# Kernel optimization log

Hardware: AMD Instinct MI355X
Metric: run time of the kernel (lower is better)

Reference implementation:

```python
import jax, jax.numpy as jnp
import numpy as np

B, T, HID = 2, 2048, 2048
NH, NKV = 16, 8
NOPE, ROPE = 128, 64
HD = NOPE + ROPE  # 192
VD = 128
KV_RANK, Q_RANK = 512, 1536
EPS = 1e-6
THETA = 10000.0
GROUPS = NH // NKV


def rmsnorm(x, w):
    var = jnp.mean(x * x, axis=-1, keepdims=True)
    return x * jax.lax.rsqrt(var + EPS) * w


def rope_cos_sin(seq_len, dtype):
    inv_freq = 1.0 / (THETA ** (jnp.arange(0, ROPE, 2, dtype=jnp.float32) / ROPE))
    t = jnp.arange(seq_len, dtype=jnp.float32)
    freqs = jnp.outer(t, inv_freq)
    emb = jnp.concatenate([freqs, freqs], axis=-1)  # [T, ROPE]
    return jnp.cos(emb).astype(dtype)[None, :, None, :], jnp.sin(emb).astype(dtype)[None, :, None, :]


def rotate_half(x):
    x1, x2 = x[..., : x.shape[-1] // 2], x[..., x.shape[-1] // 2 :]
    return jnp.concatenate([-x2, x1], axis=-1)


def setup_inputs() -> dict:
    key = jax.random.key(0)
    ks = jax.random.split(key, 7)
    s = 0.02
    return {
        "hidden_states": jax.random.normal(ks[0], (B, T, HID), jnp.float32),
        "q_a_w": jax.random.normal(ks[1], (HID, Q_RANK), jnp.float32) * s,
        "q_a_ln_w": jnp.ones((Q_RANK,), jnp.float32),
        "q_b_w": jax.random.normal(ks[2], (Q_RANK, NH * HD), jnp.float32) * s,
        "kv_a_w": jax.random.normal(ks[3], (HID, KV_RANK + NKV * ROPE), jnp.float32) * s,
        "kv_a_ln_w": jnp.ones((KV_RANK,), jnp.float32),
        "kv_b_w": jax.random.normal(ks[4], (KV_RANK, NKV * (NOPE + VD)), jnp.float32) * s,
        "o_w": jax.random.normal(ks[5], (NH * VD, HID), jnp.float32) * s,
    }


def reference(hidden_states, q_a_w, q_a_ln_w, q_b_w, kv_a_w, kv_a_ln_w, kv_b_w, o_w):
    x = hidden_states
    # Q low-rank path: a_proj -> RMSNorm -> b_proj
    q = rmsnorm(x @ q_a_w, q_a_ln_w) @ q_b_w
    q = q.reshape(B, T, NH, HD)
    q_nope, q_rope = q[..., :NOPE], q[..., NOPE:]
    # KV low-rank + decoupled rope key
    kv_raw = x @ kv_a_w
    kv_latent = rmsnorm(kv_raw[..., :KV_RANK], kv_a_ln_w)
    k_rope = kv_raw[..., KV_RANK:].reshape(B, T, NKV, ROPE)
    kv = (kv_latent @ kv_b_w).reshape(B, T, NKV, NOPE + VD)
    k_nope, v = kv[..., :NOPE], kv[..., NOPE:]
    # partial RoPE on rope slice only
    cos, sin = rope_cos_sin(T, x.dtype)
    q_rope = q_rope * cos + rotate_half(q_rope) * sin
    k_rope = k_rope * cos + rotate_half(k_rope) * sin
    q_full = jnp.concatenate([q_nope, q_rope], axis=-1)  # [B,T,NH,HD]
    k_full = jnp.concatenate([k_nope, k_rope], axis=-1)  # [B,T,NKV,HD]
    # GQA expansion (repeat_interleave over head dim)
    k_full = jnp.repeat(k_full, GROUPS, axis=2)  # [B,T,NH,HD]
    v_full = jnp.repeat(v, GROUPS, axis=2)       # [B,T,NH,VD]
    scale = HD ** -0.5
    scores = jnp.einsum("bqhd,bkhd->bhqk", q_full, k_full) * scale
    probs = jax.nn.softmax(scores, axis=-1)
    attn = jnp.einsum("bhqk,bkhd->bqhd", probs, v_full)
    out = attn.reshape(B, T, NH * VD) @ o_w
    return out
```

## Files before the change

kernel.cpp:

```cpp
#include <hip/hip_runtime.h>

using u16 = unsigned short;
using u32 = unsigned int;

typedef float f32x4 __attribute__((ext_vector_type(4)));
typedef __bf16 bf16x8 __attribute__((ext_vector_type(8)));
typedef u32 u32x2 __attribute__((ext_vector_type(2)));

__device__ __forceinline__ u16 f2bf(float f){
  u32 u = __builtin_bit_cast(u32, f);
  u32 r = (u + 0x7fffu + ((u >> 16) & 1u)) >> 16;
  return (u16)r;
}
__device__ __forceinline__ float bf2f(u16 h){
  u32 u = ((u32)h) << 16;
  return __builtin_bit_cast(float, u);
}
__device__ __forceinline__ void gl2lds16(const void* g, void* l){
  __builtin_amdgcn_global_load_lds((const __attribute__((address_space(1))) u32*)g,
                                   (__attribute__((address_space(3))) u32*)l, 16, 0, 0);
}
__device__ __forceinline__ int swz24(int ck, int r){ return (ck & 24) | ((ck ^ r) & 7); }
__device__ __forceinline__ u32 cvtpk_bf16(float a, float b){
  u32 r; asm("v_cvt_pk_bf16_f32 %0, %1, %2" : "=v"(r) : "v"(a), "v"(b)); return r;
}
__device__ __forceinline__ void mfma16(f32x4& acc, u32x2 a, u32x2 b){
  asm("v_mfma_f32_16x16x16_bf16 %0, %1, %2, %0" : "+v"(acc) : "v"(a), "v"(b));
}

__global__ __launch_bounds__(256) void cvt_f32_bf16(const float* __restrict__ in,
                                                    u16* __restrict__ out, long n){
  long i = ((long)blockIdx.x*256 + threadIdx.x)*4;
  if (i >= n) return;
  float4 v = *(const float4*)(in + i);
  u16 o[4] = { f2bf(v.x), f2bf(v.y), f2bf(v.z), f2bf(v.w) };
  *(ushort4*)(out + i) = *(ushort4*)o;
}

__global__ __launch_bounds__(256) void transpose_w(const float* __restrict__ in,
                                                   u16* __restrict__ out, int K, int N){
  __shared__ float tile[32][33];
  int n0 = blockIdx.x*32, k0 = blockIdx.y*32;
  int tx = threadIdx.x, ty = threadIdx.y;
  for (int i = ty; i < 32; i += 8)
    tile[i][tx] = in[(size_t)(k0+i)*N + n0+tx];
  __syncthreads();
  for (int i = ty; i < 32; i += 8)
    out[(size_t)(n0+i)*K + k0+tx] = f2bf(tile[tx][i]);
}

__global__ __launch_bounds__(256) void rope_tables(float* __restrict__ cosT, float* __restrict__ sinT){
  int idx = blockIdx.x*256 + threadIdx.x;
  int t = idx >> 5, d = idx & 31;
  double inv = pow(10000.0, -(double)d / 32.0);
  double a = (double)t * inv;
  cosT[idx] = (float)cos(a);
  sinT[idx] = (float)sin(a);
}

template<int OUT_BF16>
__global__ __launch_bounds__(256) void gemm_bt(const u16* __restrict__ A,
                                               const u16* __restrict__ Bt,
                                               void* __restrict__ Cout,
                                               int M, int N, int K, float cscale){
  __shared__ u16 As[128*32];
  __shared__ u16 Bs[128*32];
  const int tid = threadIdx.x, lane = tid & 63, wave = tid >> 6;
  const int m0 = blockIdx.y*128, n0 = blockIdx.x*128;
  const int wm = (wave >> 1)*64, wn = (wave & 1)*64;
  const int g = lane >> 4, lr = lane & 15;
  f32x4 acc[4][4] = {};
  const int sr = (wave*2)*16 + (lane >> 2);
  const int sc = (lane & 3)*8;
  for (int k0 = 0; k0 < K; k0 += 32){
    __syncthreads();
    #pragma unroll
    for (int i = 0; i < 2; i++){
      int c = wave*2 + i;
      int r = sr + i*16;
      gl2lds16(A  + (size_t)(m0+r)*K + k0 + sc, (char*)As + c*1024);
      gl2lds16(Bt + (size_t)(n0+r)*K + k0 + sc, (char*)Bs + c*1024);
    }
    __syncthreads();
    bf16x8 af[4], bfr[4];
    #pragma unroll
    for (int mi = 0; mi < 4; mi++) af[mi]  = *reinterpret_cast<const bf16x8*>(&As[(wm+mi*16+lr)*32 + g*8]);
    #pragma unroll
    for (int ni = 0; ni < 4; ni++) bfr[ni] = *reinterpret_cast<const bf16x8*>(&Bs[(wn+ni*16+lr)*32 + g*8]);
    #pragma unroll
    for (int mi = 0; mi < 4; mi++)
      #pragma unroll
      for (int ni = 0; ni < 4; ni++)
        acc[mi][ni] = __builtin_amdgcn_mfma_f32_16x16x32_bf16(af[mi], bfr[ni], acc[mi][ni], 0,0,0);
  }
  #pragma unroll
  for (int mi = 0; mi < 4; mi++)
    #pragma unroll
    for (int ni = 0; ni < 4; ni++)
      #pragma unroll
      for (int r = 0; r < 4; r++){
        int row = m0 + wm + mi*16 + g*4 + r;
        int col = n0 + wn + ni*16 + lr;
        float v = acc[mi][ni][r];
        if (OUT_BF16) ((u16*)Cout)[(size_t)row*N + col] = f2bf(v*cscale);
        else          ((float*)Cout)[(size_t)row*N + col] = v;
      }
}

__global__ __launch_bounds__(256) void rmsnorm_kernel(const float* __restrict__ in,
                                                      const float* __restrict__ w,
                                                      u16* __restrict__ out, int ncols, int instride){
  int row = blockIdx.x;
  const float* x = in + (size_t)row*instride;
  float ss = 0.f;
  for (int c = threadIdx.x; c < ncols; c += 256){ float v = x[c]; ss += v*v; }
  #pragma unroll
  for (int m = 1; m < 64; m <<= 1) ss += __shfl_xor(ss, m, 64);
  __shared__ float p[4];
  if ((threadIdx.x & 63) == 0) p[threadIdx.x >> 6] = ss;
  __syncthreads();
  float inv = rsqrtf((p[0]+p[1]+p[2]+p[3]) / (float)ncols + 1e-6f);
  u16* o = out + (size_t)row*ncols;
  for (int c = threadIdx.x; c < ncols; c += 256) o[c] = f2bf(x[c]*inv*w[c]);
}

__global__ __launch_bounds__(256) void kv_split_kernel(const float* __restrict__ kvraw,
                                                       const float* __restrict__ lnw,
                                                       const float* __restrict__ cosT,
                                                       const float* __restrict__ sinT,
                                                       u16* __restrict__ kvlat,
                                                       u16* __restrict__ Kf){
  int row = blockIdx.x;
  int t = row & 2047, b = row >> 11;
  const float* x = kvraw + (size_t)row*2560 + 1536;
  float ss = 0.f;
  for (int c = threadIdx.x; c < 512; c += 256){ float v = x[c]; ss += v*v; }
  #pragma unroll
  for (int m = 1; m < 64; m <<= 1) ss += __shfl_xor(ss, m, 64);
  __shared__ float p[4];
  if ((threadIdx.x & 63) == 0) p[threadIdx.x >> 6] = ss;
  __syncthreads();
  float inv = rsqrtf((p[0]+p[1]+p[2]+p[3]) / 512.0f + 1e-6f);
  for (int c = threadIdx.x; c < 512; c += 256)
    kvlat[(size_t)row*512 + c] = f2bf(x[c]*inv*lnw[c]);
  int kh = threadIdx.x >> 5, dp = threadIdx.x & 31;
  float x1 = x[512 + kh*64 + dp], x2 = x[512 + kh*64 + dp + 32];
  float cv = cosT[t*32 + dp], sv = sinT[t*32 + dp];
  float o1 = x1*cv - x2*sv;
  float o2 = x2*cv + x1*sv;
  u16* kr = Kf + ((size_t)(b*8 + kh)*2048 + t)*192;
  int c1 = 128 + dp, c2 = 128 + dp + 32;
  kr[(swz24(c1 >> 3, t) << 3) | (c1 & 7)] = f2bf(o1);
  kr[(swz24(c2 >> 3, t) << 3) | (c2 & 7)] = f2bf(o2);
}

__global__ __launch_bounds__(256) void q_rope_kernel(u16* __restrict__ q,
                                                     const float* __restrict__ cosT,
                                                     const float* __restrict__ sinT){
  int idx = blockIdx.x*256 + threadIdx.x;
  int row = idx >> 9, rem = idx & 511;
  int h = rem >> 5, dp = rem & 31;
  int t = row & 2047;
  u16* pq = q + (size_t)row*3072 + h*192 + 128;
  float x1 = bf2f(pq[dp]), x2 = bf2f(pq[dp+32]);
  float cv = cosT[t*32 + dp], sv = sinT[t*32 + dp];
  pq[dp]    = f2bf(x1*cv - x2*sv);
  pq[dp+32] = f2bf(x2*cv + x1*sv);
}

__global__ __launch_bounds__(256) void knope_kernel(const u16* __restrict__ kv,
                                                    u16* __restrict__ Kf){
  int idx = blockIdx.x*256 + threadIdx.x;
  int row = idx >> 7, rem = idx & 127;
  int kh = rem >> 4, ck = rem & 15;
  int t = row & 2047, b = row >> 11;
  int ck2 = (ck & 8) | ((ck ^ t) & 7);
  uint4 v = *(const uint4*)(kv + (size_t)row*2048 + kh*256 + ck*8);
  *(uint4*)(Kf + ((size_t)(b*8 + kh)*2048 + t)*192 + ck2*8) = v;
}

__global__ __launch_bounds__(256) void v_transpose(const u16* __restrict__ kv,
                                                   u16* __restrict__ vT){
  int bid = blockIdx.x;
  int tt = bid & 31, kvh = (bid >> 5) & 7, b = bid >> 8;
  int t0 = tt*64;
  __shared__ u16 tile[64][136];
  int tid = threadIdx.x;
  #pragma unroll
  for (int i = 0; i < 4; i++){
    int c = tid + i*256;
    int r = c >> 4, ck = c & 15;
    const u16* src = kv + ((size_t)(b*2048 + t0 + r))*2048 + kvh*256 + 128 + ck*8;
    *(uint4*)&tile[r][ck*8] = *(const uint4*)src;
  }
  __syncthreads();
  #pragma unroll
  for (int i = 0; i < 4; i++){
    int c = tid + i*256;
    int vd = c >> 3, tc = c & 7;
    int stc = tc ^ (vd & 7);
    uint4 tv;
    u16* tp = (u16*)&tv;
    #pragma unroll
    for (int j = 0; j < 8; j++) tp[j] = tile[tc*8 + j][vd];
    *(uint4*)(vT + ((size_t)(b*8 + kvh)*128 + vd)*2048 + t0 + stc*8) = tv;
  }
}

__global__ __launch_bounds__(256, 3) void attn_kernel(const u16* __restrict__ Q,
                                                      const u16* __restrict__ Kf,
                                                      const u16* __restrict__ Vt,
                                                      u16* __restrict__ Oa){
  constexpr int T = 2048;
  constexpr int NT = T/64;
  __shared__ u16 Ks[64*192];
  __shared__ u16 Vs[128*64];
  const int tid = threadIdx.x, lane = tid & 63, wave = tid >> 6;
  const int g = lane >> 4, lr = lane & 15;

  const int wg = blockIdx.x;
  const int role = (wg & 7)*64 + (wg >> 3);
  const int grp = role >> 5;
  const int b = grp >> 3, kvh = grp & 7;
  const int within = role & 31;
  const int h = kvh*2 + (within >> 4);
  const int q0 = (within & 15)*128 + wave*32;

  bf16x8 aq[2][6];
  #pragma unroll
  for (int qg = 0; qg < 2; qg++){
    const u16* qrow = Q + ((size_t)b*T + q0 + qg*16 + lr)*3072 + h*192;
    #pragma unroll
    for (int kc = 0; kc < 6; kc++)
      aq[qg][kc] = *reinterpret_cast<const bf16x8*>(qrow + kc*32 + g*8);
  }
  const u16* Kbase = Kf + (size_t)(b*8 + kvh)*T*192;
  const u16* Vbase = Vt + (size_t)(b*8 + kvh)*128*T;

  f32x4 ovb[2][8] = {};
  float mq[2] = {-1e30f, -1e30f};
  float lq[2] = {0.f, 0.f};

  auto stageK = [&](int kt){
    const u16* ksrc = Kbase + (size_t)kt*12288 + wave*3072 + lane*8;
    #pragma unroll
    for (int i = 0; i < 6; i++)
      gl2lds16(ksrc + i*512, (char*)Ks + (wave*6 + i)*1024);
  };
  auto stageV = [&](int kt){
    #pragma unroll
    for (int i = 0; i < 4; i++){
      int c = wave*4 + i;
      const u16* vsrc = Vbase + (size_t)(c*8 + (lane >> 3))*T + kt*64 + (lane & 7)*8;
      gl2lds16(vsrc, (char*)Vs + c*1024);
    }
  };

  stageK(0);
  stageV(0);
  __syncthreads();

  for (int kt = 0; kt < NT; kt++){
    const bool notlast = (kt + 1 < NT);

    f32x4 s[2][4];
    __builtin_amdgcn_s_setprio(1);
    #pragma unroll
    for (int nb = 0; nb < 4; nb++){
      const int row = nb*16 + lr;
      f32x4 a0 = {0.f,0.f,0.f,0.f}, a1 = {0.f,0.f,0.f,0.f};
      #pragma unroll
      for (int kc = 0; kc < 6; kc++){
        int ckl = swz24(kc*4 + g, row);
        bf16x8 kf = *reinterpret_cast<const bf16x8*>(&Ks[row*192 + ckl*8]);
        a0 = __builtin_amdgcn_mfma_f32_16x16x32_bf16(kf, aq[0][kc], a0, 0,0,0);
        a1 = __builtin_amdgcn_mfma_f32_16x16x32_bf16(kf, aq[1][kc], a1, 0,0,0);
      }
      s[0][nb] = a0; s[1][nb] = a1;
    }
    __builtin_amdgcn_s_setprio(0);

    __syncthreads();
    if (notlast) stageK(kt + 1);

    u32 pk[2][4][2];
    #pragma unroll
    for (int qg = 0; qg < 2; qg++){
      float pm = s[qg][0][0];
      #pragma unroll
      for (int nb = 0; nb < 4; nb++)
        #pragma unroll
        for (int r = 0; r < 4; r++)
          if (nb || r) pm = fmaxf(pm, s[qg][nb][r]);
      pm = fmaxf(pm, __shfl_xor(pm, 16, 64));
      pm = fmaxf(pm, __shfl_xor(pm, 32, 64));
      if (!__all(pm <= mq[qg] + 8.f)){
        float mn = fmaxf(mq[qg], pm);
        float corr = __expf(mq[qg] - mn);
        mq[qg] = mn;
        lq[qg] *= corr;
        #pragma unroll
        for (int r = 0; r < 4; r++){
          float cr = __shfl(corr, (lane & 48) | (g*4 + r), 64);
          #pragma unroll
          for (int vb = 0; vb < 8; vb++) ovb[qg][vb][r] *= cr;
        }
      }
      float ls = 0.f;
      #pragma unroll
      for (int nb = 0; nb < 4; nb++){
        float e0 = __expf(s[qg][nb][0] - mq[qg]);
        float e1 = __expf(s[qg][nb][1] - mq[qg]);
        float e2 = __expf(s[qg][nb][2] - mq[qg]);
        float e3 = __expf(s[qg][nb][3] - mq[qg]);
        ls += (e0 + e1) + (e2 + e3);
        pk[qg][nb][0] = cvtpk_bf16(e0, e1);
        pk[qg][nb][1] = cvtpk_bf16(e2, e3);
      }
      ls += __shfl_xor(ls, 16, 64);
      ls += __shfl_xor(ls, 32, 64);
      lq[qg] += ls;
    }

    __builtin_amdgcn_s_setprio(1);
    const int vsw = lr & 7;
    #pragma unroll
    for (int vb = 0; vb < 8; vb++){
      const int vd = vb*16 + lr;
      #pragma unroll
      for (int nb = 0; nb < 4; nb++){
        int ck = (nb*2 + (g >> 1)) ^ vsw;
        u32x2 bv = *reinterpret_cast<const u32x2*>(&Vs[vd*64 + ck*8 + (g & 1)*4]);
        u32x2 pa0; pa0.x = pk[0][nb][0]; pa0.y = pk[0][nb][1];
        u32x2 pa1; pa1.x = pk[1][nb][0]; pa1.y = pk[1][nb][1];
        mfma16(ovb[0][vb], pa0, bv);
        mfma16(ovb[1][vb], pa1, bv);
      }
    }
    __builtin_amdgcn_s_setprio(0);

    if (notlast){
      __syncthreads();
      stageV(kt + 1);
    }
  }

  #pragma unroll
  for (int qg = 0; qg < 2; qg++){
    float invq = 1.0f / lq[qg];
    float inv_r[4];
    #pragma unroll
    for (int r = 0; r < 4; r++)
      inv_r[r] = __shfl(invq, (lane & 48) | (g*4 + r), 64);
    u16* obase = Oa + ((size_t)b*T + q0 + qg*16)*2048 + h*128;
    #pragma unroll
    for (int vb = 0; vb < 8; vb++)
      #pragma unroll
      for (int r = 0; r < 4; r++)
        obase[(size_t)(g*4 + r)*2048 + vb*16 + lr] = f2bf(ovb[qg][vb][r]*inv_r[r]);
  }
}

extern "C" void kernel_launch(void* const* d_in, const int* in_sizes, int n_in,
                              void* d_out, int out_size, void* d_ws, size_t ws_size,
                              hipStream_t stream){
  const float* hs      = (const float*)d_in[0];
  const float* q_a_w   = (const float*)d_in[1];
  const float* q_a_ln  = (const float*)d_in[2];
  const float* q_b_w   = (const float*)d_in[3];
  const float* kv_a_w  = (const float*)d_in[4];
  const float* kv_a_ln = (const float*)d_in[5];
  const float* kv_b_w  = (const float*)d_in[6];
  const float* o_w     = (const float*)d_in[7];

  char* ws = (char*)d_ws;
  size_t off = 0;
  auto alloc = [&](size_t bytes){ void* p = ws + off; off += bytes; return p; };
  u16*  Wqa   = (u16*)alloc(1536ull*2048*2);
  u16*  Wkva  = (u16*)alloc(1024ull*2048*2);
  u16*  Wqb   = (u16*)alloc(3072ull*1536*2);
  u16*  Wkvb  = (u16*)alloc(2048ull*512*2);
  u16*  Wo    = (u16*)alloc(2048ull*2048*2);
  u16*  XB    = (u16*)alloc(4096ull*2048*2);
  char* R23   = (char*)alloc(4096ull*2560*4);
  u16*  Qlat  = (u16*)alloc(4096ull*1536*2);
  u16*  KVlat = (u16*)alloc(4096ull*512*2);
  u16*  Kf    = (u16*)alloc(2ull*8*2048*192*2);
  u16*  Vt    = (u16*)alloc(2ull*8*128*2048*2);
  float* cosT = (float*)alloc(2048ull*32*4);
  float* sinT = (float*)alloc(2048ull*32*4);
  (void)ws_size; (void)in_sizes; (void)n_in; (void)out_size;

  u16* QB  = (u16*)R23;
  u16* KVB = (u16*)(R23 + 4096ull*3072*2);

  const float qscale = 0.07216878364870322f;

  cvt_f32_bf16<<<8192, 256, 0, stream>>>(hs, XB, 4096ll*2048);
  transpose_w<<<dim3(1536/32, 2048/32), dim3(32,8), 0, stream>>>(q_a_w,  Wqa,  2048, 1536);
  transpose_w<<<dim3(1024/32, 2048/32), dim3(32,8), 0, stream>>>(kv_a_w, Wkva, 2048, 1024);
  transpose_w<<<dim3(3072/32, 1536/32), dim3(32,8), 0, stream>>>(q_b_w,  Wqb,  1536, 3072);
  transpose_w<<<dim3(2048/32,  512/32), dim3(32,8), 0, stream>>>(kv_b_w, Wkvb,  512, 2048);
  transpose_w<<<dim3(2048/32, 2048/32), dim3(32,8), 0, stream>>>(o_w,    Wo,   2048, 2048);
  rope_tables<<<256, 256, 0, stream>>>(cosT, sinT);

  gemm_bt<0><<<dim3(20, 32), 256, 0, stream>>>(XB, Wqa, (float*)R23, 4096, 2560, 2048, 1.0f);
  rmsnorm_kernel<<<4096, 256, 0, stream>>>((const float*)R23, q_a_ln, Qlat, 1536, 2560);
  kv_split_kernel<<<4096, 256, 0, stream>>>((const float*)R23, kv_a_ln, cosT, sinT, KVlat, Kf);
  gemm_bt<1><<<dim3(24, 32), 256, 0, stream>>>(Qlat, Wqb, QB, 4096, 3072, 1536, qscale);
  q_rope_kernel<<<8192, 256, 0, stream>>>(QB, cosT, sinT);
  gemm_bt<1><<<dim3(16, 32), 256, 0, stream>>>(KVlat, Wkvb, KVB, 4096, 2048, 512, 1.0f);
  knope_kernel<<<2048, 256, 0, stream>>>(KVB, Kf);
  v_transpose<<<512, 256, 0, stream>>>(KVB, Vt);
  attn_kernel<<<512, 256, 0, stream>>>(QB, Kf, Vt, XB);
  gemm_bt<0><<<dim3(16, 32), 256, 0, stream>>>(XB, Wo, (float*)d_out, 4096, 2048, 2048, 1.0f);
}
```

Baseline: 416.4 us.

## Double-buffer V tiles and use 16x16x32 MFMA for PV via LDS P staging

Result: faster. 371.4 us (-10.8%).

```diff
diff --git a/kernel.cpp b/kernel.cpp
--- a/kernel.cpp
+++ b/kernel.cpp
@@ -5,7 +5,6 @@
 
 typedef float f32x4 __attribute__((ext_vector_type(4)));
 typedef __bf16 bf16x8 __attribute__((ext_vector_type(8)));
-typedef u32 u32x2 __attribute__((ext_vector_type(2)));
 
 __device__ __forceinline__ u16 f2bf(float f){
   u32 u = __builtin_bit_cast(u32, f);
@@ -23,9 +22,6 @@
 __device__ __forceinline__ int swz24(int ck, int r){ return (ck & 24) | ((ck ^ r) & 7); }
 __device__ __forceinline__ u32 cvtpk_bf16(float a, float b){
   u32 r; asm("v_cvt_pk_bf16_f32 %0, %1, %2" : "=v"(r) : "v"(a), "v"(b)); return r;
-}
-__device__ __forceinline__ void mfma16(f32x4& acc, u32x2 a, u32x2 b){
-  asm("v_mfma_f32_16x16x16_bf16 %0, %1, %2, %0" : "+v"(acc) : "v"(a), "v"(b));
 }
 
 __global__ __launch_bounds__(256) void cvt_f32_bf16(const float* __restrict__ in,
@@ -207,14 +203,15 @@
   }
 }
 
-__global__ __launch_bounds__(256, 3) void attn_kernel(const u16* __restrict__ Q,
+__global__ __launch_bounds__(256, 2) void attn_kernel(const u16* __restrict__ Q,
                                                       const u16* __restrict__ Kf,
                                                       const u16* __restrict__ Vt,
                                                       u16* __restrict__ Oa){
   constexpr int T = 2048;
   constexpr int NT = T/64;
   __shared__ u16 Ks[64*192];
-  __shared__ u16 Vs[128*64];
+  __shared__ u16 Vs[2][128*64];
+  __shared__ u16 Ps[4][2048];
   const int tid = threadIdx.x, lane = tid & 63, wave = tid >> 6;
   const int g = lane >> 4, lr = lane & 15;
 
@@ -247,21 +244,24 @@
     for (int i = 0; i < 6; i++)
       gl2lds16(ksrc + i*512, (char*)Ks + (wave*6 + i)*1024);
   };
-  auto stageV = [&](int kt){
+  auto stageV = [&](int kt, int buf){
     #pragma unroll
     for (int i = 0; i < 4; i++){
       int c = wave*4 + i;
       const u16* vsrc = Vbase + (size_t)(c*8 + (lane >> 3))*T + kt*64 + (lane & 7)*8;
-      gl2lds16(vsrc, (char*)Vs + c*1024);
+      gl2lds16(vsrc, (char*)(&Vs[0][0]) + buf*16384 + c*1024);
     }
   };
 
   stageK(0);
-  stageV(0);
+  stageV(0, 0);
   __syncthreads();
 
+  int buf = 0;
   for (int kt = 0; kt < NT; kt++){
     const bool notlast = (kt + 1 < NT);
+
+    if (notlast) stageV(kt + 1, buf ^ 1);
 
     f32x4 s[2][4];
     __builtin_amdgcn_s_setprio(1);
@@ -280,10 +280,11 @@
     }
     __builtin_amdgcn_s_setprio(0);
 
-    __syncthreads();
+    asm volatile("s_waitcnt lgkmcnt(0)" ::: "memory");
+    __builtin_amdgcn_s_barrier();
+    __builtin_amdgcn_sched_barrier(0);
     if (notlast) stageK(kt + 1);
 
-    u32 pk[2][4][2];
     #pragma unroll
     for (int qg = 0; qg < 2; qg++){
       float pm = s[qg][0][0];
@@ -314,35 +315,42 @@
         float e2 = __expf(s[qg][nb][2] - mq[qg]);
         float e3 = __expf(s[qg][nb][3] - mq[qg]);
         ls += (e0 + e1) + (e2 + e3);
-        pk[qg][nb][0] = cvtpk_bf16(e0, e1);
-        pk[qg][nb][1] = cvtpk_bf16(e2, e3);
+        int stc = (2*nb + (g >> 1)) ^ (lr & 7);
+        volatile u32* p = (volatile u32*)&Ps[wave][qg*1024 + lr*64 + stc*8 + (g & 1)*4];
+        p[0] = cvtpk_bf16(e0, e1);
+        p[1] = cvtpk_bf16(e2, e3);
       }
       ls += __shfl_xor(ls, 16, 64);
       ls += __shfl_xor(ls, 32, 64);
       lq[qg] += ls;
     }
 
+    asm volatile("s_waitcnt lgkmcnt(0)" ::: "memory");
+    __builtin_amdgcn_sched_barrier(0);
+
+    bf16x8 ap[2][2];
+    #pragma unroll
+    for (int qg = 0; qg < 2; qg++)
+      #pragma unroll
+      for (int k2 = 0; k2 < 2; k2++){
+        int ck = (k2*4 + g) ^ (lr & 7);
+        ap[qg][k2] = *reinterpret_cast<const bf16x8*>(&Ps[wave][qg*1024 + lr*64 + ck*8]);
+      }
     __builtin_amdgcn_s_setprio(1);
-    const int vsw = lr & 7;
-    #pragma unroll
-    for (int vb = 0; vb < 8; vb++){
-      const int vd = vb*16 + lr;
-      #pragma unroll
-      for (int nb = 0; nb < 4; nb++){
-        int ck = (nb*2 + (g >> 1)) ^ vsw;
-        u32x2 bv = *reinterpret_cast<const u32x2*>(&Vs[vd*64 + ck*8 + (g & 1)*4]);
-        u32x2 pa0; pa0.x = pk[0][nb][0]; pa0.y = pk[0][nb][1];
-        u32x2 pa1; pa1.x = pk[1][nb][0]; pa1.y = pk[1][nb][1];
-        mfma16(ovb[0][vb], pa0, bv);
-        mfma16(ovb[1][vb], pa1, bv);
-      }
-    }
+    #pragma unroll
+    for (int vb = 0; vb < 8; vb++)
+      #pragma unroll
+      for (int k2 = 0; k2 < 2; k2++){
+        int vd = vb*16 + lr;
+        int ck = (k2*4 + g) ^ (vd & 7);
+        bf16x8 bv = *reinterpret_cast<const bf16x8*>(&Vs[buf][vd*64 + ck*8]);
+        ovb[0][vb] = __builtin_amdgcn_mfma_f32_16x16x32_bf16(ap[0][k2], bv, ovb[0][vb], 0,0,0);
+        ovb[1][vb] = __builtin_amdgcn_mfma_f32_16x16x32_bf16(ap[1][k2], bv, ovb[1][vb], 0,0,0);
+      }
     __builtin_amdgcn_s_setprio(0);
 
-    if (notlast){
-      __syncthreads();
-      stageV(kt + 1);
-    }
+    if (notlast) __syncthreads();
+    buf ^= 1;
   }
 
   #pragma unroll
```
